# Performance work log

Measured on AMD Instinct MI355X. Metric: run time of the kernel, lower is better.

Reference implementation:

```python
import jax, jax.numpy as jnp
import numpy as np

NEG = -10000.0
START, STOP = 3, 4
NTAGS = 5
T, V, E, H = 2048, 100000, 512, 1024
Hh = H // 2


def setup_inputs() -> dict:
    key = jax.random.key(0)
    ks = jax.random.split(key, 12)
    s = 0.05
    sentence = jax.random.randint(ks[0], (T,), 0, V)
    emb = jax.random.normal(ks[1], (V, E), dtype=jnp.float32) * s
    w_ih_f = jax.random.normal(ks[2], (4 * Hh, E), dtype=jnp.float32) * s
    w_hh_f = jax.random.normal(ks[3], (4 * Hh, Hh), dtype=jnp.float32) * s
    b_f = jnp.zeros((4 * Hh,), dtype=jnp.float32)
    w_ih_b = jax.random.normal(ks[4], (4 * Hh, E), dtype=jnp.float32) * s
    w_hh_b = jax.random.normal(ks[5], (4 * Hh, Hh), dtype=jnp.float32) * s
    b_b = jnp.zeros((4 * Hh,), dtype=jnp.float32)
    w_out = jax.random.normal(ks[6], (NTAGS, H), dtype=jnp.float32) * s
    b_out = jnp.zeros((NTAGS,), dtype=jnp.float32)
    transitions = jax.random.normal(ks[7], (NTAGS, NTAGS), dtype=jnp.float32)
    transitions = transitions.at[START, :].set(NEG).at[:, STOP].set(NEG)
    h0 = jax.random.normal(ks[8], (2, 1, Hh), dtype=jnp.float32)
    c0 = jax.random.normal(ks[9], (2, 1, Hh), dtype=jnp.float32)
    return dict(sentence=sentence, emb=emb, w_ih_f=w_ih_f, w_hh_f=w_hh_f, b_f=b_f,
                w_ih_b=w_ih_b, w_hh_b=w_hh_b, b_b=b_b, w_out=w_out, b_out=b_out,
                transitions=transitions, h0=h0, c0=c0)


def _lstm_dir(x, h, c, w_ih, w_hh, b):
    # x: [T, E]; h, c: [Hh]. PyTorch gate order: i, f, g, o.
    def step(carry, xt):
        h, c = carry
        g = xt @ w_ih.T + h @ w_hh.T + b  # [4*Hh]
        i, f, gg, o = jnp.split(g, 4)
        i = jax.nn.sigmoid(i)
        f = jax.nn.sigmoid(f)
        gg = jnp.tanh(gg)
        o = jax.nn.sigmoid(o)
        c = f * c + i * gg
        h = o * jnp.tanh(c)
        return (h, c), h
    _, hs = jax.lax.scan(step, (h, c), x)
    return hs  # [T, Hh]


def _crf_forward(feats, transitions):
    # feats: [T, NTAGS]. Vectorized CRF forward algorithm (log partition).
    fv0 = jnp.full((NTAGS,), NEG, dtype=feats.dtype).at[START].set(0.0)
    def step(fv, feat):
        # next_tag_var[j, i] = fv[i] + transitions[j, i] + feat[j]
        fv = jax.nn.logsumexp(fv[None, :] + transitions + feat[:, None], axis=1)
        return fv, None
    fv, _ = jax.lax.scan(step, fv0, feats)
    return jax.nn.logsumexp(fv + transitions[STOP])


def reference(sentence, emb, w_ih_f, w_hh_f, b_f, w_ih_b, w_hh_b, b_b,
              w_out, b_out, transitions, h0, c0):
    x = emb[sentence]  # [T, E]
    hf = _lstm_dir(x, h0[0, 0], c0[0, 0], w_ih_f, w_hh_f, b_f)
    hb = _lstm_dir(x[::-1], h0[1, 0], c0[1, 0], w_ih_b, w_hh_b, b_b)[::-1]
    lstm_out = jnp.concatenate([hf, hb], axis=-1)  # [T, H]
    feats = lstm_out @ w_out.T + b_out  # [T, NTAGS]
    return _crf_forward(feats, transitions)
```

## Files before the change

kernel.cpp:

```cpp
#include <hip/hip_runtime.h>
#include <hip/hip_bf16.h>
#include <math.h>

#define TT 2048
#define EE 512
#define HH 512
#define G4 2048
#define NTAGS 5
#define START_TAG 3
#define STOP_TAG 4
#define NEGV -10000.0f

#define BM 128
#define BN 128
#define BK 16

__global__ __launch_bounds__(256) void gemm_ih_kernel(
    const int* __restrict__ sent, const float* __restrict__ emb,
    const float* __restrict__ w, const float* __restrict__ bias,
    float* __restrict__ G)
{
    __shared__ float As[BK][BM + 4];
    __shared__ float Bs[BK][BN + 4];
    const int tid = threadIdx.x;
    const int t0 = blockIdx.y * BM;
    const int n0 = blockIdx.x * BN;
    const int lrow = tid >> 1;
    const int lk   = (tid & 1) * 8;
    const float* ap = emb + (long)sent[t0 + lrow] * EE + lk;
    const float* bp = w + (long)(n0 + lrow) * EE + lk;
    const int ty = tid >> 4, tx = tid & 15;

    float acc[8][8];
#pragma unroll
    for (int i = 0; i < 8; ++i)
#pragma unroll
        for (int j = 0; j < 8; ++j) acc[i][j] = 0.f;

    for (int k = 0; k < EE; k += BK) {
        float4 a0 = *(const float4*)(ap + k);
        float4 a1 = *(const float4*)(ap + k + 4);
        float4 b0 = *(const float4*)(bp + k);
        float4 b1 = *(const float4*)(bp + k + 4);
        __syncthreads();
        As[lk+0][lrow]=a0.x; As[lk+1][lrow]=a0.y; As[lk+2][lrow]=a0.z; As[lk+3][lrow]=a0.w;
        As[lk+4][lrow]=a1.x; As[lk+5][lrow]=a1.y; As[lk+6][lrow]=a1.z; As[lk+7][lrow]=a1.w;
        Bs[lk+0][lrow]=b0.x; Bs[lk+1][lrow]=b0.y; Bs[lk+2][lrow]=b0.z; Bs[lk+3][lrow]=b0.w;
        Bs[lk+4][lrow]=b1.x; Bs[lk+5][lrow]=b1.y; Bs[lk+6][lrow]=b1.z; Bs[lk+7][lrow]=b1.w;
        __syncthreads();
#pragma unroll
        for (int kk = 0; kk < BK; ++kk) {
            float a[8], b[8];
            *(float4*)&a[0] = *(const float4*)&As[kk][ty*8];
            *(float4*)&a[4] = *(const float4*)&As[kk][ty*8 + 4];
            *(float4*)&b[0] = *(const float4*)&Bs[kk][tx*8];
            *(float4*)&b[4] = *(const float4*)&Bs[kk][tx*8 + 4];
#pragma unroll
            for (int i = 0; i < 8; ++i)
#pragma unroll
                for (int j = 0; j < 8; ++j) acc[i][j] += a[i] * b[j];
        }
    }
    float bv[8];
#pragma unroll
    for (int j = 0; j < 8; ++j) bv[j] = bias[n0 + tx*8 + j];
#pragma unroll
    for (int i = 0; i < 8; ++i) {
        const long t = t0 + ty*8 + i;
        float4 o0 = make_float4(acc[i][0]+bv[0], acc[i][1]+bv[1], acc[i][2]+bv[2], acc[i][3]+bv[3]);
        float4 o1 = make_float4(acc[i][4]+bv[4], acc[i][5]+bv[5], acc[i][6]+bv[6], acc[i][7]+bv[7]);
        *(float4*)&G[t*G4 + n0 + tx*8]     = o0;
        *(float4*)&G[t*G4 + n0 + tx*8 + 4] = o1;
    }
}

__device__ __forceinline__ unsigned long long pack_ht(unsigned int tag, float v) {
    return ((unsigned long long)tag << 32) | (unsigned long long)__float_as_uint(v);
}

__global__ void init_kernel(const float* __restrict__ h0,
                            unsigned long long* __restrict__ htag)
{
    for (int i = threadIdx.x; i < 2 * HH; i += 256) {
        const int dir = i >> 9, k = i & 511;
        htag[(dir * 2 + 0) * HH + k] = pack_ht(0u, h0[i]);
        htag[(dir * 2 + 1) * HH + k] = pack_ht(0xFFFFFFFFu, 0.f);
    }
}

__device__ __forceinline__ float fast_tanh(float x) {
    const float ax = fabsf(x);
    const float z = __expf(-2.f * ax);
    const float t = (1.f - z) / (1.f + z);
    return copysignf(t, x);
}

#define NB 32

__global__ __launch_bounds__(256, 1) void lstm_rec_kernel(
    const float* __restrict__ Gf, const float* __restrict__ Gb,
    const float* __restrict__ whh_f, const float* __restrict__ whh_b,
    const float* __restrict__ c0,
    unsigned long long* __restrict__ htag, float* __restrict__ hs)
{
    const int dir = blockIdx.x >> 5;
    const int blk = blockIdx.x & 31;
    const int tid = threadIdx.x;
    const int kg  = tid & 15;
    const int e   = tid >> 4;
    const int row = blk * 16 + e;
    const float* whh = dir ? whh_b : whh_f;
    const float* Gd  = dir ? Gb : Gf;
    unsigned long long* hslots = htag + (long)dir * 2 * HH;

    float4 w[4][8];
#pragma unroll
    for (int g = 0; g < 4; ++g) {
        const float* wr = whh + (long)(g * HH + row) * HH + kg * 32;
#pragma unroll
        for (int v = 0; v < 8; ++v) w[g][v] = *(const float4*)(wr + v * 4);
    }
#pragma unroll
    for (int g = 0; g < 4; ++g)
#pragma unroll
        for (int v = 0; v < 8; ++v)
            asm volatile("" : "+v"(w[g][v].x), "+v"(w[g][v].y),
                              "+v"(w[g][v].z), "+v"(w[g][v].w));

    float c = c0[dir * HH + row];

    __shared__ float hl[2][HH + 64];

    float gc[4] = {0.f,0.f,0.f,0.f}, gn[4];
    if (kg == 0) {
        const int trow = dir ? (TT - 1) : 0;
#pragma unroll
        for (int g = 0; g < 4; ++g) gc[g] = Gd[(long)trow * G4 + g * HH + row];
    }

    const int i0 = tid * 2;
    const int pi = i0 + ((i0 >> 5) << 2);
    const int pb = kg * 36;

    for (int t = 0; t < TT; ++t) {
        const int p = t & 1;
        const unsigned int tagv = (unsigned int)t;
        unsigned long long* slot = hslots + p * HH;

        if (kg == 0) {
            const int tn = (t + 1 < TT) ? (t + 1) : t;
            const int trow = dir ? (TT - 1 - tn) : tn;
#pragma unroll
            for (int g = 0; g < 4; ++g) gn[g] = Gd[(long)trow * G4 + g * HH + row];
        }

        unsigned long long a0 = __hip_atomic_load(&slot[i0],   __ATOMIC_RELAXED, __HIP_MEMORY_SCOPE_AGENT);
        unsigned long long a1 = __hip_atomic_load(&slot[i0+1], __ATOMIC_RELAXED, __HIP_MEMORY_SCOPE_AGENT);
        while (((unsigned int)(a0 >> 32) != tagv) | ((unsigned int)(a1 >> 32) != tagv)) {
            __builtin_amdgcn_s_sleep(1);
            a0 = __hip_atomic_load(&slot[i0],   __ATOMIC_RELAXED, __HIP_MEMORY_SCOPE_AGENT);
            a1 = __hip_atomic_load(&slot[i0+1], __ATOMIC_RELAXED, __HIP_MEMORY_SCOPE_AGENT);
        }
        hl[p][pi]     = __uint_as_float((unsigned int)a0);
        hl[p][pi + 1] = __uint_as_float((unsigned int)a1);

        __syncthreads();

        float4 h4[8];
#pragma unroll
        for (int i = 0; i < 8; ++i) h4[i] = *(const float4*)&hl[p][pb + i * 4];

        float acc[4];
#pragma unroll
        for (int g = 0; g < 4; ++g) {
            float s = 0.f;
#pragma unroll
            for (int v = 0; v < 8; ++v)
                s += w[g][v].x*h4[v].x + w[g][v].y*h4[v].y + w[g][v].z*h4[v].z + w[g][v].w*h4[v].w;
            acc[g] = s;
        }
#pragma unroll
        for (int m = 1; m < 16; m <<= 1) {
#pragma unroll
            for (int g = 0; g < 4; ++g) acc[g] += __shfl_xor(acc[g], m);
        }

        if (kg == 0) {
            const float xi = acc[0] + gc[0];
            const float xf = acc[1] + gc[1];
            const float xg = acc[2] + gc[2];
            const float xo = acc[3] + gc[3];
            const float si = 1.f / (1.f + __expf(-xi));
            const float sf = 1.f / (1.f + __expf(-xf));
            const float sg = fast_tanh(xg);
            const float so = 1.f / (1.f + __expf(-xo));
            c = sf * c + si * sg;
            const float h = so * fast_tanh(c);
            const int trow = dir ? (TT - 1 - t) : t;
            hs[((long)dir * TT + trow) * HH + row] = h;
            __hip_atomic_store(&hslots[((t + 1) & 1) * HH + row],
                               pack_ht((unsigned int)(t + 1), h),
                               __ATOMIC_RELAXED, __HIP_MEMORY_SCOPE_AGENT);
            gc[0]=gn[0]; gc[1]=gn[1]; gc[2]=gn[2]; gc[3]=gn[3];
        }
    }
}

__global__ __launch_bounds__(64) void feats_kernel(
    const float* __restrict__ hs, const float* __restrict__ w_out,
    const float* __restrict__ b_out, float* __restrict__ feats)
{
    const int t = blockIdx.x;
    const int lane = threadIdx.x;
    const float* src = (lane < 32) ? (hs + (long)t * HH + lane * 16)
                                   : (hs + (long)(TT + t) * HH + (lane - 32) * 16);
    float x[16];
#pragma unroll
    for (int i = 0; i < 4; ++i) *(float4*)&x[i*4] = *(const float4*)(src + i*4);
    const int kglob = lane * 16;
    float pj[NTAGS];
#pragma unroll
    for (int j = 0; j < NTAGS; ++j) {
        const float* wr = w_out + (long)j * 1024 + kglob;
        float s = 0.f;
#pragma unroll
        for (int i = 0; i < 4; ++i) {
            float4 wv = *(const float4*)(wr + i*4);
            s += wv.x*x[i*4] + wv.y*x[i*4+1] + wv.z*x[i*4+2] + wv.w*x[i*4+3];
        }
        pj[j] = s;
    }
#pragma unroll
    for (int m = 1; m < 64; m <<= 1) {
#pragma unroll
        for (int j = 0; j < NTAGS; ++j) pj[j] += __shfl_xor(pj[j], m);
    }
    if (lane == 0) {
#pragma unroll
        for (int j = 0; j < NTAGS; ++j) feats[(long)t * NTAGS + j] = pj[j] + b_out[j];
    }
}

__global__ __launch_bounds__(64) void crf_kernel(
    const float* __restrict__ feats, const float* __restrict__ trans,
    float* __restrict__ out)
{
    __shared__ float fl[TT * NTAGS];
    const int lane = threadIdx.x;
    for (int i = lane; i < TT * NTAGS; i += 64) fl[i] = feats[i];
    __syncthreads();

    const int j = (lane < NTAGS) ? lane : 0;
    float tr[NTAGS];
#pragma unroll
    for (int i = 0; i < NTAGS; ++i) tr[i] = trans[j * NTAGS + i];
    float fv = (j == START_TAG) ? 0.f : NEGV;

    for (int t = 0; t < TT; ++t) {
        const float x0 = __shfl(fv, 0) + tr[0];
        const float x1 = __shfl(fv, 1) + tr[1];
        const float x2 = __shfl(fv, 2) + tr[2];
        const float x3 = __shfl(fv, 3) + tr[3];
        const float x4 = __shfl(fv, 4) + tr[4];
        const float m = fmaxf(fmaxf(fmaxf(x0, x1), fmaxf(x2, x3)), x4);
        const float s = expf(x0-m) + expf(x1-m) + expf(x2-m) + expf(x3-m) + expf(x4-m);
        fv = fl[t * NTAGS + j] + m + logf(s);
    }
    const float xx = fv + trans[STOP_TAG * NTAGS + j];
    const float y0 = __shfl(xx, 0), y1 = __shfl(xx, 1), y2 = __shfl(xx, 2),
                y3 = __shfl(xx, 3), y4 = __shfl(xx, 4);
    if (lane == 0) {
        const float m = fmaxf(fmaxf(fmaxf(y0, y1), fmaxf(y2, y3)), y4);
        const float s = expf(y0-m) + expf(y1-m) + expf(y2-m) + expf(y3-m) + expf(y4-m);
        out[0] = m + logf(s);
    }
}

extern "C" void kernel_launch(void* const* d_in, const int* in_sizes, int n_in,
                              void* d_out, int out_size, void* d_ws, size_t ws_size,
                              hipStream_t stream)
{
    (void)in_sizes; (void)n_in; (void)out_size; (void)ws_size;
    const int*   sent  = (const int*)d_in[0];
    const float* emb   = (const float*)d_in[1];
    const float* wihf  = (const float*)d_in[2];
    const float* whhf  = (const float*)d_in[3];
    const float* bf    = (const float*)d_in[4];
    const float* wihb  = (const float*)d_in[5];
    const float* whhb  = (const float*)d_in[6];
    const float* bb    = (const float*)d_in[7];
    const float* wout  = (const float*)d_in[8];
    const float* bout  = (const float*)d_in[9];
    const float* trans = (const float*)d_in[10];
    const float* h0    = (const float*)d_in[11];
    const float* c0    = (const float*)d_in[12];
    float* out = (float*)d_out;

    char* ws = (char*)d_ws;
    float* Gf    = (float*)(ws);
    float* Gb    = (float*)(ws + 16777216);
    float* hs    = (float*)(ws + 33554432);
    float* feats = (float*)(ws + 41943040);
    unsigned long long* htag = (unsigned long long*)(ws + 42000384);

    init_kernel<<<1, 256, 0, stream>>>(h0, htag);
    gemm_ih_kernel<<<dim3(G4 / BN, TT / BM), 256, 0, stream>>>(sent, emb, wihf, bf, Gf);
    gemm_ih_kernel<<<dim3(G4 / BN, TT / BM), 256, 0, stream>>>(sent, emb, wihb, bb, Gb);
    lstm_rec_kernel<<<2 * NB, 256, 0, stream>>>(Gf, Gb, whhf, whhb, c0, htag, hs);
    feats_kernel<<<TT, 64, 0, stream>>>(hs, wout, bout, feats);
    crf_kernel<<<1, 64, 0, stream>>>(feats, trans, out);
}
```

Baseline: 5.237 ms.

## Make LSTM recurrence wave-local and merge the two input-projection GEMMs

The recurrent kernel is reorganised so that each wavefront owns four hidden rows. Each lane reads its eight h values directly from the global tagged slots, which removes the LDS staging and the per-step __syncthreads. The reduction now runs as a 64-lane shuffle over 16 accumulators, and the hidden-state store is issued before the hs write to shorten the critical path. The forward and backward input GEMMs are merged into one launch using blockIdx.z. In exchange, each lane does more polling loads per step and the shuffle reduction is longer.

```diff
diff --git a/kernel.cpp b/kernel.cpp
--- a/kernel.cpp
+++ b/kernel.cpp
@@ -15,11 +15,16 @@
 #define BN 128
 #define BK 16
 
-__global__ __launch_bounds__(256) void gemm_ih_kernel(
+__global__ __launch_bounds__(256) void gemm_ih2_kernel(
     const int* __restrict__ sent, const float* __restrict__ emb,
-    const float* __restrict__ w, const float* __restrict__ bias,
-    float* __restrict__ G)
-{
+    const float* __restrict__ wf, const float* __restrict__ bf,
+    const float* __restrict__ wb, const float* __restrict__ bb,
+    float* __restrict__ Gf, float* __restrict__ Gb)
+{
+    const float* w    = blockIdx.z ? wb : wf;
+    const float* bias = blockIdx.z ? bb : bf;
+    float*       G    = blockIdx.z ? Gb : Gf;
+
     __shared__ float As[BK][BM + 4];
     __shared__ float Bs[BK][BN + 4];
     const int tid = threadIdx.x;
@@ -95,8 +100,6 @@
     return copysignf(t, x);
 }
 
-#define NB 32
-
 __global__ __launch_bounds__(256, 1) void lstm_rec_kernel(
     const float* __restrict__ Gf, const float* __restrict__ Gb,
     const float* __restrict__ whh_f, const float* __restrict__ whh_b,
@@ -106,101 +109,118 @@
     const int dir = blockIdx.x >> 5;
     const int blk = blockIdx.x & 31;
     const int tid = threadIdx.x;
-    const int kg  = tid & 15;
-    const int e   = tid >> 4;
-    const int row = blk * 16 + e;
+    const int lane = tid & 63;
+    const int wv   = blk * 4 + (tid >> 6);
+    const int rowbase = wv * 4;
+    const int rg = lane & 3;
+    const int kg = lane >> 2;
+    const int ks = kg * 32 + rg * 8;
     const float* whh = dir ? whh_b : whh_f;
     const float* Gd  = dir ? Gb : Gf;
     unsigned long long* hslots = htag + (long)dir * 2 * HH;
 
-    float4 w[4][8];
-#pragma unroll
-    for (int g = 0; g < 4; ++g) {
-        const float* wr = whh + (long)(g * HH + row) * HH + kg * 32;
-#pragma unroll
-        for (int v = 0; v < 8; ++v) w[g][v] = *(const float4*)(wr + v * 4);
-    }
-#pragma unroll
-    for (int g = 0; g < 4; ++g)
-#pragma unroll
-        for (int v = 0; v < 8; ++v)
-            asm volatile("" : "+v"(w[g][v].x), "+v"(w[g][v].y),
-                              "+v"(w[g][v].z), "+v"(w[g][v].w));
-
-    float c = c0[dir * HH + row];
-
-    __shared__ float hl[2][HH + 64];
-
-    float gc[4] = {0.f,0.f,0.f,0.f}, gn[4];
-    if (kg == 0) {
+    float4 w4[4][4][2];
+#pragma unroll
+    for (int r = 0; r < 4; ++r)
+#pragma unroll
+        for (int g = 0; g < 4; ++g) {
+            const float* wr = whh + (long)(g * HH + rowbase + r) * HH + ks;
+            w4[r][g][0] = *(const float4*)(wr);
+            w4[r][g][1] = *(const float4*)(wr + 4);
+        }
+#pragma unroll
+    for (int r = 0; r < 4; ++r)
+#pragma unroll
+        for (int g = 0; g < 4; ++g)
+#pragma unroll
+            for (int v = 0; v < 2; ++v)
+                asm volatile("" : "+v"(w4[r][g][v].x), "+v"(w4[r][g][v].y),
+                                  "+v"(w4[r][g][v].z), "+v"(w4[r][g][v].w));
+
+    float c = 0.f;
+    float gc[4] = {0.f,0.f,0.f,0.f}, gn[4] = {0.f,0.f,0.f,0.f};
+    if (lane < 4) {
+        c = c0[dir * HH + rowbase + lane];
         const int trow = dir ? (TT - 1) : 0;
 #pragma unroll
-        for (int g = 0; g < 4; ++g) gc[g] = Gd[(long)trow * G4 + g * HH + row];
-    }
-
-    const int i0 = tid * 2;
-    const int pi = i0 + ((i0 >> 5) << 2);
-    const int pb = kg * 36;
+        for (int g = 0; g < 4; ++g) gc[g] = Gd[(long)trow * G4 + g * HH + rowbase + lane];
+    }
 
     for (int t = 0; t < TT; ++t) {
         const int p = t & 1;
         const unsigned int tagv = (unsigned int)t;
         unsigned long long* slot = hslots + p * HH;
 
-        if (kg == 0) {
+        if (lane < 4) {
             const int tn = (t + 1 < TT) ? (t + 1) : t;
             const int trow = dir ? (TT - 1 - tn) : tn;
 #pragma unroll
-            for (int g = 0; g < 4; ++g) gn[g] = Gd[(long)trow * G4 + g * HH + row];
-        }
-
-        unsigned long long a0 = __hip_atomic_load(&slot[i0],   __ATOMIC_RELAXED, __HIP_MEMORY_SCOPE_AGENT);
-        unsigned long long a1 = __hip_atomic_load(&slot[i0+1], __ATOMIC_RELAXED, __HIP_MEMORY_SCOPE_AGENT);
-        while (((unsigned int)(a0 >> 32) != tagv) | ((unsigned int)(a1 >> 32) != tagv)) {
+            for (int g = 0; g < 4; ++g) gn[g] = Gd[(long)trow * G4 + g * HH + rowbase + lane];
+        }
+
+        unsigned long long a[8];
+#pragma unroll
+        for (int j = 0; j < 8; ++j)
+            a[j] = __hip_atomic_load(&slot[ks + j], __ATOMIC_RELAXED, __HIP_MEMORY_SCOPE_AGENT);
+        for (;;) {
+            bool ok = true;
+#pragma unroll
+            for (int j = 0; j < 8; ++j) ok &= ((unsigned int)(a[j] >> 32) == tagv);
+            if (ok) break;
             __builtin_amdgcn_s_sleep(1);
-            a0 = __hip_atomic_load(&slot[i0],   __ATOMIC_RELAXED, __HIP_MEMORY_SCOPE_AGENT);
-            a1 = __hip_atomic_load(&slot[i0+1], __ATOMIC_RELAXED, __HIP_MEMORY_SCOPE_AGENT);
-        }
-        hl[p][pi]     = __uint_as_float((unsigned int)a0);
-        hl[p][pi + 1] = __uint_as_float((unsigned int)a1);
-
-        __syncthreads();
-
-        float4 h4[8];
-#pragma unroll
-        for (int i = 0; i < 8; ++i) h4[i] = *(const float4*)&hl[p][pb + i * 4];
-
-        float acc[4];
-#pragma unroll
-        for (int g = 0; g < 4; ++g) {
-            float s = 0.f;
-#pragma unroll
-            for (int v = 0; v < 8; ++v)
-                s += w[g][v].x*h4[v].x + w[g][v].y*h4[v].y + w[g][v].z*h4[v].z + w[g][v].w*h4[v].w;
-            acc[g] = s;
-        }
-#pragma unroll
-        for (int m = 1; m < 16; m <<= 1) {
-#pragma unroll
-            for (int g = 0; g < 4; ++g) acc[g] += __shfl_xor(acc[g], m);
-        }
-
-        if (kg == 0) {
-            const float xi = acc[0] + gc[0];
-            const float xf = acc[1] + gc[1];
-            const float xg = acc[2] + gc[2];
-            const float xo = acc[3] + gc[3];
+#pragma unroll
+            for (int j = 0; j < 8; ++j)
+                a[j] = __hip_atomic_load(&slot[ks + j], __ATOMIC_RELAXED, __HIP_MEMORY_SCOPE_AGENT);
+        }
+        float h[8];
+#pragma unroll
+        for (int j = 0; j < 8; ++j) h[j] = __uint_as_float((unsigned int)a[j]);
+
+        float acc[4][4];
+#pragma unroll
+        for (int r = 0; r < 4; ++r)
+#pragma unroll
+            for (int g = 0; g < 4; ++g) {
+                const float4 w0 = w4[r][g][0], w1 = w4[r][g][1];
+                acc[r][g] = w0.x*h[0] + w0.y*h[1] + w0.z*h[2] + w0.w*h[3]
+                          + w1.x*h[4] + w1.y*h[5] + w1.z*h[6] + w1.w*h[7];
+            }
+
+#pragma unroll
+        for (int m = 1; m < 64; m <<= 1) {
+#pragma unroll
+            for (int r = 0; r < 4; ++r)
+#pragma unroll
+                for (int g = 0; g < 4; ++g)
+                    acc[r][g] += __shfl_xor(acc[r][g], m);
+        }
+
+        if (lane < 4) {
+            float xv[4];
+#pragma unroll
+            for (int g = 0; g < 4; ++g) {
+                float v = acc[0][g];
+                v = (lane == 1) ? acc[1][g] : v;
+                v = (lane == 2) ? acc[2][g] : v;
+                v = (lane == 3) ? acc[3][g] : v;
+                xv[g] = v;
+            }
+            const float xi = xv[0] + gc[0];
+            const float xf = xv[1] + gc[1];
+            const float xg = xv[2] + gc[2];
+            const float xo = xv[3] + gc[3];
             const float si = 1.f / (1.f + __expf(-xi));
             const float sf = 1.f / (1.f + __expf(-xf));
             const float sg = fast_tanh(xg);
             const float so = 1.f / (1.f + __expf(-xo));
             c = sf * c + si * sg;
-            const float h = so * fast_tanh(c);
+            const float h_new = so * fast_tanh(c);
+            const int row = rowbase + lane;
+            __hip_atomic_store(&hslots[((t + 1) & 1) * HH + row],
+                               pack_ht((unsigned int)(t + 1), h_new),
+                               __ATOMIC_RELAXED, __HIP_MEMORY_SCOPE_AGENT);
             const int trow = dir ? (TT - 1 - t) : t;
-            hs[((long)dir * TT + trow) * HH + row] = h;
-            __hip_atomic_store(&hslots[((t + 1) & 1) * HH + row],
-                               pack_ht((unsigned int)(t + 1), h),
-                               __ATOMIC_RELAXED, __HIP_MEMORY_SCOPE_AGENT);
+            hs[((long)dir * TT + trow) * HH + row] = h_new;
             gc[0]=gn[0]; gc[1]=gn[1]; gc[2]=gn[2]; gc[3]=gn[3];
         }
     }
@@ -304,9 +324,9 @@
     unsigned long long* htag = (unsigned long long*)(ws + 42000384);
 
     init_kernel<<<1, 256, 0, stream>>>(h0, htag);
-    gemm_ih_kernel<<<dim3(G4 / BN, TT / BM), 256, 0, stream>>>(sent, emb, wihf, bf, Gf);
-    gemm_ih_kernel<<<dim3(G4 / BN, TT / BM), 256, 0, stream>>>(sent, emb, wihb, bb, Gb);
-    lstm_rec_kernel<<<2 * NB, 256, 0, stream>>>(Gf, Gb, whhf, whhb, c0, htag, hs);
+    gemm_ih2_kernel<<<dim3(G4 / BN, TT / BM, 2), 256, 0, stream>>>(
+        sent, emb, wihf, bf, wihb, bb, Gf, Gb);
+    lstm_rec_kernel<<<64, 256, 0, stream>>>(Gf, Gb, whhf, whhb, c0, htag, hs);
     feats_kernel<<<TT, 64, 0, stream>>>(hs, wout, bout, feats);
     crf_kernel<<<1, 64, 0, stream>>>(feats, trans, out);
 }
```

Result: slower. 9.820 ms (+87.5%).
